# Kernel tuning notes

Hardware: AMD Instinct MI355X
Metric: run time of the kernel (lower is better)

Reference implementation:

```python
import jax, jax.numpy as jnp
import numpy as np

INPUT_SIZE = 128
OUTPUT_SIZE = 32
LIFTING_DIM = 512
BATCH = 32768


def setup_inputs() -> dict:
    key = jax.random.key(0)
    ks = jax.random.split(key, 7)
    x = jax.random.normal(ks[0], (BATCH, INPUT_SIZE), dtype=jnp.float32)
    # Linear(input_size, lifting_dim) with bias (torch layout: W [out, in])
    lim1 = 1.0 / np.sqrt(INPUT_SIZE)
    W1 = jax.random.uniform(ks[1], (LIFTING_DIM, INPUT_SIZE), jnp.float32, -lim1, lim1)
    b1 = jax.random.uniform(ks[2], (LIFTING_DIM,), jnp.float32, -lim1, lim1)
    # Linear(lifting_dim, output_size, bias=False)
    lim2 = 1.0 / np.sqrt(LIFTING_DIM)
    W2 = jax.random.uniform(ks[3], (OUTPUT_SIZE, LIFTING_DIM), jnp.float32, -lim2, lim2)
    # Quadratic params: L_vars ~ randn, b ~ randn, c ~ randn (as in module init)
    n_tril = LIFTING_DIM * (LIFTING_DIM + 1) // 2
    L_vars = jax.random.normal(ks[4], (n_tril,), dtype=jnp.float32)
    qb = jax.random.normal(ks[5], (LIFTING_DIM,), dtype=jnp.float32)
    qc = jax.random.normal(ks[6], (1,), dtype=jnp.float32)
    return {"x": x, "W1": W1, "b1": b1, "W2": W2, "L_vars": L_vars, "qb": qb, "qc": qc}


def reference(x, W1, b1, W2, L_vars, qb, qc):
    # lifting: phi = tanh(x @ W1^T + b1)   [B, lifting_dim]
    phi = jnp.tanh(x @ W1.T + b1)
    # actor: linear feedback (no bias)     [B, output_size]
    pi = phi @ W2.T
    # critic: quadratic form y = phi' Q phi + b' phi + c with Q = L L^T (PSD)
    rows, cols = jnp.tril_indices(LIFTING_DIM)  # row-major, same order as torch.tril_indices
    L = jnp.zeros((LIFTING_DIM, LIFTING_DIM), dtype=L_vars.dtype).at[rows, cols].set(L_vars)
    Q = L @ L.T
    # diag(phi @ Q @ phi.T) == sum((phi @ Q) * phi, axis=1)  -- O(B*d^2), same math
    y = jnp.sum((phi @ Q) * phi, axis=1) + phi @ qb + qc  # [B]
    vf = y[:, None]  # [B, 1]
    return pi, vf
```

## Files before the change

kernel.cpp:

```cpp
#include <hip/hip_runtime.h>
#include <hip/hip_bf16.h>
#include <stdint.h>

typedef short bf16x8 __attribute__((ext_vector_type(8)));
typedef float f32x4 __attribute__((ext_vector_type(4)));

#define DEVI static __device__ __forceinline__

constexpr int B_   = 32768;
constexpr int IN_  = 128;
constexpr int LF_  = 512;
constexpr int OUT_ = 32;
constexpr int NE_  = 48;

constexpr size_t OFF_XB  = 0;
constexpr size_t OFF_LT  = 8388608;
constexpr size_t OFF_W1  = OFF_LT + 524288;
constexpr size_t OFF_W2E = OFF_W1 + 131072;

DEVI void gl2lds16(const void* g, void* l) {
    __builtin_amdgcn_global_load_lds(
        (const __attribute__((address_space(1))) unsigned int*)g,
        (__attribute__((address_space(3))) unsigned int*)l,
        16, 0, 0);
}

DEVI bf16x8 frag4(const char* base, int row, int kofs) {
    int c = ((kofs >> 3) & 3) ^ (row & 3);
    return *(const bf16x8*)(base + (size_t)((row << 2) + c) * 16);
}
DEVI bf16x8 phiFrag(const char* p, int row, int kofs) {
    int c = (kofs >> 3) ^ (row & 7);
    return *(const bf16x8*)(p + (size_t)((row << 6) + c) * 16);
}
DEVI void phiStore(char* p, int row, int col, __hip_bfloat16 v) {
    int c = (col >> 3) ^ (row & 7);
    *(__hip_bfloat16*)(p + (size_t)((row << 6) + c) * 16 + (col & 7) * 2) = v;
}

__global__ __launch_bounds__(256) void k_prep(
        const float* __restrict__ x,  const float* __restrict__ w1,
        const float* __restrict__ w2, const float* __restrict__ lv,
        const float* __restrict__ qb,
        __hip_bfloat16* __restrict__ xb, __hip_bfloat16* __restrict__ w1b,
        __hip_bfloat16* __restrict__ lt, __hip_bfloat16* __restrict__ w2e) {
    int gt = blockIdx.x * blockDim.x + threadIdx.x;
    int st = gridDim.x * blockDim.x;
    for (int i = gt; i < B_ * IN_; i += st) xb[i] = __float2bfloat16(x[i]);
    for (int i = gt; i < LF_ * IN_; i += st) w1b[i] = __float2bfloat16(w1[i]);
    for (int i = gt; i < NE_ * LF_; i += st) {
        int n = i >> 9, k = i & 511;
        float v = (n < OUT_) ? w2[n * LF_ + k] : (n == OUT_ ? qb[k] : 0.f);
        w2e[i] = __float2bfloat16(v);
    }
    for (int i = gt; i < LF_ * LF_; i += st) {
        int j = i >> 9, k = i & 511;
        float v = (k >= j) ? lv[k * (k + 1) / 2 + j] : 0.f;
        lt[i] = __float2bfloat16(v);
    }
}

__global__ __launch_bounds__(256, 2) void k_fused(
        const __hip_bfloat16* __restrict__ xb, const __hip_bfloat16* __restrict__ w1b,
        const float* __restrict__ b1, const __hip_bfloat16* __restrict__ w2e,
        const __hip_bfloat16* __restrict__ lt, const float* __restrict__ qcp,
        float* __restrict__ pi, float* __restrict__ vf) {
    __shared__ char smem[79104];
    char*  phiB   = smem;
    char*  stageA = smem + 65536;
    char*  stageB = smem + 69632;
    float* vfb    = (float*)(smem + 77824);
    float* vfp    = (float*)(smem + 78080);

    const int tid = threadIdx.x, wv = tid >> 6, ln = tid & 63;
    const int cl = ln & 15, q = ln >> 4;
    const int m0 = blockIdx.x * 64;

    {
        const int wm = (wv & 1) * 32, wn = (wv >> 1) * 64;
        for (int n0 = 0; n0 < LF_; n0 += 128) {
            f32x4 acc[2][4] = {};
            for (int k0 = 0; k0 < IN_; k0 += 32) {
                __syncthreads();
                {
                    int slot = tid, row = slot >> 2, c = (slot & 3) ^ (row & 3);
                    gl2lds16(xb + (size_t)(m0 + row) * IN_ + k0 + c * 8,
                             stageA + (size_t)(wv * 64) * 16);
                }
#pragma unroll
                for (int it = 0; it < 2; ++it) {
                    int slot = it * 256 + tid, row = slot >> 2, c = (slot & 3) ^ (row & 3);
                    gl2lds16(w1b + (size_t)(n0 + row) * IN_ + k0 + c * 8,
                             stageB + (size_t)(it * 256 + wv * 64) * 16);
                }
                __syncthreads();
                bf16x8 af[2], bfr[4];
#pragma unroll
                for (int i = 0; i < 2; ++i) af[i]  = frag4(stageA, wm + i * 16 + cl, q * 8);
#pragma unroll
                for (int i = 0; i < 4; ++i) bfr[i] = frag4(stageB, wn + i * 16 + cl, q * 8);
#pragma unroll
                for (int mi = 0; mi < 2; ++mi)
#pragma unroll
                    for (int ni = 0; ni < 4; ++ni)
                        acc[mi][ni] = __builtin_amdgcn_mfma_f32_16x16x32_bf16(
                            af[mi], bfr[ni], acc[mi][ni], 0, 0, 0);
            }
#pragma unroll
            for (int ni = 0; ni < 4; ++ni) {
                int colg = n0 + wn + ni * 16 + cl;
                float bv = b1[colg];
#pragma unroll
                for (int mi = 0; mi < 2; ++mi)
#pragma unroll
                    for (int r = 0; r < 4; ++r) {
                        int row = wm + mi * 16 + q * 4 + r;
                        phiStore(phiB, row, colg,
                                 __float2bfloat16(tanhf(acc[mi][ni][r] + bv)));
                    }
            }
        }
    }
    __syncthreads();

    {
        const int wm = wv * 16;
        f32x4 a2[3] = {};
        for (int k0 = 0; k0 < LF_; k0 += 32) {
            bf16x8 a = phiFrag(phiB, wm + cl, k0 + q * 8);
#pragma unroll
            for (int ni = 0; ni < 3; ++ni) {
                bf16x8 b = *(const bf16x8*)(w2e + (size_t)(ni * 16 + cl) * LF_ + k0 + q * 8);
                a2[ni] = __builtin_amdgcn_mfma_f32_16x16x32_bf16(a, b, a2[ni], 0, 0, 0);
            }
        }
#pragma unroll
        for (int ni = 0; ni < 3; ++ni)
#pragma unroll
            for (int r = 0; r < 4; ++r) {
                int row = wm + q * 4 + r, col = ni * 16 + cl;
                float v = a2[ni][r];
                if (col < OUT_)       pi[(size_t)(m0 + row) * OUT_ + col] = v;
                else if (col == OUT_) vfb[row] = v;
            }
    }

    {
        const int wn = wv * 32;
        float vacc[4][4] = {};
        for (int n0 = 0; n0 < LF_; n0 += 128) {
            f32x4 acc[4][2] = {};
            for (int k0 = n0; k0 < LF_; k0 += 32) {
                __syncthreads();
#pragma unroll
                for (int it = 0; it < 2; ++it) {
                    int slot = it * 256 + tid, row = slot >> 2, c = (slot & 3) ^ (row & 3);
                    gl2lds16(lt + (size_t)(n0 + row) * LF_ + k0 + c * 8,
                             stageB + (size_t)(it * 256 + wv * 64) * 16);
                }
                __syncthreads();
                bf16x8 bfr[2];
#pragma unroll
                for (int ni = 0; ni < 2; ++ni) bfr[ni] = frag4(stageB, wn + ni * 16 + cl, q * 8);
#pragma unroll
                for (int mi = 0; mi < 4; ++mi) {
                    bf16x8 a = phiFrag(phiB, mi * 16 + cl, k0 + q * 8);
#pragma unroll
                    for (int ni = 0; ni < 2; ++ni)
                        acc[mi][ni] = __builtin_amdgcn_mfma_f32_16x16x32_bf16(
                            a, bfr[ni], acc[mi][ni], 0, 0, 0);
                }
            }
#pragma unroll
            for (int mi = 0; mi < 4; ++mi)
#pragma unroll
                for (int r = 0; r < 4; ++r) {
                    float s = 0.f;
#pragma unroll
                    for (int ni = 0; ni < 2; ++ni) { float t = acc[mi][ni][r]; s += t * t; }
                    vacc[mi][r] += s;
                }
        }
#pragma unroll
        for (int mi = 0; mi < 4; ++mi)
#pragma unroll
            for (int r = 0; r < 4; ++r) {
                float v = vacc[mi][r];
                v += __shfl_xor(v, 1, 64);
                v += __shfl_xor(v, 2, 64);
                v += __shfl_xor(v, 4, 64);
                v += __shfl_xor(v, 8, 64);
                vacc[mi][r] = v;
            }
        if (cl == 0)
#pragma unroll
            for (int mi = 0; mi < 4; ++mi)
#pragma unroll
                for (int r = 0; r < 4; ++r)
                    vfp[wv * 64 + mi * 16 + q * 4 + r] = vacc[mi][r];
    }
    __syncthreads();
    if (tid < 64) {
        float v = vfb[tid] + qcp[0] +
                  vfp[tid] + vfp[64 + tid] + vfp[128 + tid] + vfp[192 + tid];
        vf[m0 + tid] = v;
    }
}

extern "C" void kernel_launch(void* const* d_in, const int* in_sizes, int n_in,
                              void* d_out, int out_size, void* d_ws, size_t ws_size,
                              hipStream_t stream) {
    const float* x  = (const float*)d_in[0];
    const float* w1 = (const float*)d_in[1];
    const float* b1 = (const float*)d_in[2];
    const float* w2 = (const float*)d_in[3];
    const float* lv = (const float*)d_in[4];
    const float* qb = (const float*)d_in[5];
    const float* qc = (const float*)d_in[6];

    char* ws = (char*)d_ws;
    __hip_bfloat16* xb  = (__hip_bfloat16*)(ws + OFF_XB);
    __hip_bfloat16* lt  = (__hip_bfloat16*)(ws + OFF_LT);
    __hip_bfloat16* w1b = (__hip_bfloat16*)(ws + OFF_W1);
    __hip_bfloat16* w2e = (__hip_bfloat16*)(ws + OFF_W2E);

    float* pi = (float*)d_out;
    float* vf = pi + (size_t)B_ * OUT_;

    k_prep <<<1024, 256, 0, stream>>>(x, w1, w2, lv, qb, xb, w1b, lt, w2e);
    k_fused<<<B_ / 64, 256, 0, stream>>>(xb, w1b, b1, w2e, lt, qc, pi, vf);
}
```

Baseline: 128.2 us.

## Fuse x bf16 conversion into main kernel, drop LDS staging, rebalance triangular GEMM

The fp32-to-bf16 conversion of x now happens inside the fused kernel, which removes the 8 MB bf16 round-trip and shrinks the prep kernel to weights only. The prep kernel transposes L through a shared-memory tile so its reads and writes are coalesced. In the fused kernel the W1 and L operands are read straight from global/L2 into registers rather than staged through LDS with barriers, so most of the per-k __syncthreads are gone. Triangular tiles are dealt to waves in paired order to balance work, and tanh uses an exp/rcp approximation. The risks are more global-load latency exposed without LDS staging, and a small accuracy loss from the approximate tanh.

```diff
diff --git a/kernel.cpp b/kernel.cpp
--- a/kernel.cpp
+++ b/kernel.cpp
@@ -13,111 +13,124 @@
 constexpr int OUT_ = 32;
 constexpr int NE_  = 48;
 
-constexpr size_t OFF_XB  = 0;
-constexpr size_t OFF_LT  = 8388608;
-constexpr size_t OFF_W1  = OFF_LT + 524288;
+constexpr size_t OFF_LT  = 0;
+constexpr size_t OFF_W1  = 524288;
 constexpr size_t OFF_W2E = OFF_W1 + 131072;
 
-DEVI void gl2lds16(const void* g, void* l) {
-    __builtin_amdgcn_global_load_lds(
-        (const __attribute__((address_space(1))) unsigned int*)g,
-        (__attribute__((address_space(3))) unsigned int*)l,
-        16, 0, 0);
-}
-
-DEVI bf16x8 frag4(const char* base, int row, int kofs) {
-    int c = ((kofs >> 3) & 3) ^ (row & 3);
-    return *(const bf16x8*)(base + (size_t)((row << 2) + c) * 16);
-}
+DEVI short f2bs(float f) { __hip_bfloat16 h = __float2bfloat16(f); return *(short*)&h; }
+
+DEVI float tanh_fast(float v) {
+    float e = __expf(2.0f * v);
+    return 1.0f - 2.0f * __builtin_amdgcn_rcpf(e + 1.0f);
+}
+
 DEVI bf16x8 phiFrag(const char* p, int row, int kofs) {
     int c = (kofs >> 3) ^ (row & 7);
     return *(const bf16x8*)(p + (size_t)((row << 6) + c) * 16);
 }
-DEVI void phiStore(char* p, int row, int col, __hip_bfloat16 v) {
+DEVI void phiStore(char* p, int row, int col, float v) {
     int c = (col >> 3) ^ (row & 7);
-    *(__hip_bfloat16*)(p + (size_t)((row << 6) + c) * 16 + (col & 7) * 2) = v;
+    *(short*)(p + (size_t)((row << 6) + c) * 16 + (col & 7) * 2) = f2bs(v);
+}
+DEVI bf16x8 xFrag(const char* p, int row, int kofs) {
+    int c = (kofs >> 3) ^ (row & 15);
+    return *(const bf16x8*)(p + (size_t)((row << 4) + c) * 16);
 }
 
 __global__ __launch_bounds__(256) void k_prep(
-        const float* __restrict__ x,  const float* __restrict__ w1,
-        const float* __restrict__ w2, const float* __restrict__ lv,
-        const float* __restrict__ qb,
-        __hip_bfloat16* __restrict__ xb, __hip_bfloat16* __restrict__ w1b,
-        __hip_bfloat16* __restrict__ lt, __hip_bfloat16* __restrict__ w2e) {
-    int gt = blockIdx.x * blockDim.x + threadIdx.x;
-    int st = gridDim.x * blockDim.x;
-    for (int i = gt; i < B_ * IN_; i += st) xb[i] = __float2bfloat16(x[i]);
-    for (int i = gt; i < LF_ * IN_; i += st) w1b[i] = __float2bfloat16(w1[i]);
-    for (int i = gt; i < NE_ * LF_; i += st) {
-        int n = i >> 9, k = i & 511;
-        float v = (n < OUT_) ? w2[n * LF_ + k] : (n == OUT_ ? qb[k] : 0.f);
-        w2e[i] = __float2bfloat16(v);
-    }
-    for (int i = gt; i < LF_ * LF_; i += st) {
-        int j = i >> 9, k = i & 511;
-        float v = (k >= j) ? lv[k * (k + 1) / 2 + j] : 0.f;
-        lt[i] = __float2bfloat16(v);
+        const float* __restrict__ w1, const float* __restrict__ w2,
+        const float* __restrict__ lv, const float* __restrict__ qb,
+        __hip_bfloat16* __restrict__ w1b, __hip_bfloat16* __restrict__ lt,
+        __hip_bfloat16* __restrict__ w2e) {
+    int b = blockIdx.x, tid = threadIdx.x;
+    if (b < 64) {
+        __shared__ float tbuf[64][65];
+        int bj = b >> 3, bk = b & 7;
+        for (int i = tid; i < 4096; i += 256) {
+            int kk = i >> 6, jj = i & 63;
+            int k = bk * 64 + kk, j = bj * 64 + jj;
+            tbuf[kk][jj] = (k >= j) ? lv[k * (k + 1) / 2 + j] : 0.f;
+        }
+        __syncthreads();
+        for (int i = tid; i < 4096; i += 256) {
+            int jj = i >> 6, kk = i & 63;
+            lt[(size_t)(bj * 64 + jj) * LF_ + bk * 64 + kk] = __float2bfloat16(tbuf[kk][jj]);
+        }
+    } else if (b < 96) {
+        int gt = (b - 64) * 256 + tid;
+        for (int i = gt; i < LF_ * IN_ / 4; i += 8192) {
+            float4 v = ((const float4*)w1)[i];
+            short4 s = { f2bs(v.x), f2bs(v.y), f2bs(v.z), f2bs(v.w) };
+            ((short4*)w1b)[i] = s;
+        }
+    } else {
+        int gt = (b - 96) * 256 + tid;
+        for (int i = gt; i < NE_ * LF_; i += 8192) {
+            int n = i >> 9, k = i & 511;
+            float v = (n < OUT_) ? w2[n * LF_ + k] : (n == OUT_ ? qb[k] : 0.f);
+            w2e[i] = __float2bfloat16(v);
+        }
     }
 }
 
 __global__ __launch_bounds__(256, 2) void k_fused(
-        const __hip_bfloat16* __restrict__ xb, const __hip_bfloat16* __restrict__ w1b,
+        const float* __restrict__ x, const __hip_bfloat16* __restrict__ w1b,
         const float* __restrict__ b1, const __hip_bfloat16* __restrict__ w2e,
         const __hip_bfloat16* __restrict__ lt, const float* __restrict__ qcp,
         float* __restrict__ pi, float* __restrict__ vf) {
-    __shared__ char smem[79104];
-    char*  phiB   = smem;
-    char*  stageA = smem + 65536;
-    char*  stageB = smem + 69632;
-    float* vfb    = (float*)(smem + 77824);
-    float* vfp    = (float*)(smem + 78080);
+    __shared__ char smem[81920];
+    char*  phiB  = smem;
+    char*  stage = smem + 65536;
+    float* vfb   = (float*)stage;
+    float* vfp   = (float*)(stage + 256);
 
     const int tid = threadIdx.x, wv = tid >> 6, ln = tid & 63;
     const int cl = ln & 15, q = ln >> 4;
     const int m0 = blockIdx.x * 64;
 
+#pragma unroll
+    for (int it = 0; it < 4; ++it) {
+        int slot = it * 256 + tid, row = slot >> 4, cg = slot & 15;
+        const float4* p = (const float4*)(x + (size_t)(m0 + row) * IN_ + cg * 8);
+        float4 u0 = p[0], u1 = p[1];
+        bf16x8 pk;
+        pk[0] = f2bs(u0.x); pk[1] = f2bs(u0.y); pk[2] = f2bs(u0.z); pk[3] = f2bs(u0.w);
+        pk[4] = f2bs(u1.x); pk[5] = f2bs(u1.y); pk[6] = f2bs(u1.z); pk[7] = f2bs(u1.w);
+        *(bf16x8*)(stage + (size_t)((row << 4) + (cg ^ (row & 15))) * 16) = pk;
+    }
+    __syncthreads();
+
     {
-        const int wm = (wv & 1) * 32, wn = (wv >> 1) * 64;
-        for (int n0 = 0; n0 < LF_; n0 += 128) {
-            f32x4 acc[2][4] = {};
+        const int n0w = wv * 128;
+#pragma unroll
+        for (int ch = 0; ch < 2; ++ch) {
+            f32x4 acc[4][4] = {};
+#pragma unroll
             for (int k0 = 0; k0 < IN_; k0 += 32) {
-                __syncthreads();
-                {
-                    int slot = tid, row = slot >> 2, c = (slot & 3) ^ (row & 3);
-                    gl2lds16(xb + (size_t)(m0 + row) * IN_ + k0 + c * 8,
-                             stageA + (size_t)(wv * 64) * 16);
-                }
-#pragma unroll
-                for (int it = 0; it < 2; ++it) {
-                    int slot = it * 256 + tid, row = slot >> 2, c = (slot & 3) ^ (row & 3);
-                    gl2lds16(w1b + (size_t)(n0 + row) * IN_ + k0 + c * 8,
-                             stageB + (size_t)(it * 256 + wv * 64) * 16);
-                }
-                __syncthreads();
-                bf16x8 af[2], bfr[4];
-#pragma unroll
-                for (int i = 0; i < 2; ++i) af[i]  = frag4(stageA, wm + i * 16 + cl, q * 8);
-#pragma unroll
-                for (int i = 0; i < 4; ++i) bfr[i] = frag4(stageB, wn + i * 16 + cl, q * 8);
-#pragma unroll
-                for (int mi = 0; mi < 2; ++mi)
+                bf16x8 a[4], bfr[4];
+#pragma unroll
+                for (int mi = 0; mi < 4; ++mi) a[mi] = xFrag(stage, mi * 16 + cl, k0 + q * 8);
+#pragma unroll
+                for (int ni = 0; ni < 4; ++ni)
+                    bfr[ni] = *(const bf16x8*)(
+                        w1b + (size_t)(n0w + ch * 64 + ni * 16 + cl) * IN_ + k0 + q * 8);
+#pragma unroll
+                for (int mi = 0; mi < 4; ++mi)
 #pragma unroll
                     for (int ni = 0; ni < 4; ++ni)
                         acc[mi][ni] = __builtin_amdgcn_mfma_f32_16x16x32_bf16(
-                            af[mi], bfr[ni], acc[mi][ni], 0, 0, 0);
+                            a[mi], bfr[ni], acc[mi][ni], 0, 0, 0);
             }
 #pragma unroll
             for (int ni = 0; ni < 4; ++ni) {
-                int colg = n0 + wn + ni * 16 + cl;
+                int colg = n0w + ch * 64 + ni * 16 + cl;
                 float bv = b1[colg];
 #pragma unroll
-                for (int mi = 0; mi < 2; ++mi)
-#pragma unroll
-                    for (int r = 0; r < 4; ++r) {
-                        int row = wm + mi * 16 + q * 4 + r;
-                        phiStore(phiB, row, colg,
-                                 __float2bfloat16(tanhf(acc[mi][ni][r] + bv)));
-                    }
+                for (int mi = 0; mi < 4; ++mi)
+#pragma unroll
+                    for (int r = 0; r < 4; ++r)
+                        phiStore(phiB, mi * 16 + q * 4 + r, colg,
+                                 tanh_fast(acc[mi][ni][r] + bv));
             }
         }
     }
@@ -146,40 +159,40 @@
     }
 
     {
-        const int wn = wv * 32;
         float vacc[4][4] = {};
-        for (int n0 = 0; n0 < LF_; n0 += 128) {
-            f32x4 acc[4][2] = {};
-            for (int k0 = n0; k0 < LF_; k0 += 32) {
-                __syncthreads();
-#pragma unroll
-                for (int it = 0; it < 2; ++it) {
-                    int slot = it * 256 + tid, row = slot >> 2, c = (slot & 3) ^ (row & 3);
-                    gl2lds16(lt + (size_t)(n0 + row) * LF_ + k0 + c * 8,
-                             stageB + (size_t)(it * 256 + wv * 64) * 16);
+#pragma unroll
+        for (int s = 0; s < 2; ++s) {
+            int tl[4] = { 16 * s + wv, 16 * s + 7 - wv, 16 * s + 8 + wv, 16 * s + 15 - wv };
+            int ks[4];
+#pragma unroll
+            for (int j = 0; j < 4; ++j) ks[j] = (tl[j] * 16) & ~31;
+            int kmin = min(min(ks[0], ks[1]), min(ks[2], ks[3]));
+            f32x4 acc[4][4] = {};
+            for (int k0 = kmin; k0 < LF_; k0 += 32) {
+                bf16x8 a[4];
+#pragma unroll
+                for (int mi = 0; mi < 4; ++mi) a[mi] = phiFrag(phiB, mi * 16 + cl, k0 + q * 8);
+#pragma unroll
+                for (int j = 0; j < 4; ++j) {
+                    if (k0 >= ks[j]) {
+                        bf16x8 b = *(const bf16x8*)(
+                            lt + (size_t)(tl[j] * 16 + cl) * LF_ + k0 + q * 8);
+#pragma unroll
+                        for (int mi = 0; mi < 4; ++mi)
+                            acc[j][mi] = __builtin_amdgcn_mfma_f32_16x16x32_bf16(
+                                a[mi], b, acc[j][mi], 0, 0, 0);
+                    }
                 }
-                __syncthreads();
-                bf16x8 bfr[2];
-#pragma unroll
-                for (int ni = 0; ni < 2; ++ni) bfr[ni] = frag4(stageB, wn + ni * 16 + cl, q * 8);
-#pragma unroll
-                for (int mi = 0; mi < 4; ++mi) {
-                    bf16x8 a = phiFrag(phiB, mi * 16 + cl, k0 + q * 8);
-#pragma unroll
-                    for (int ni = 0; ni < 2; ++ni)
-                        acc[mi][ni] = __builtin_amdgcn_mfma_f32_16x16x32_bf16(
-                            a, bfr[ni], acc[mi][ni], 0, 0, 0);
-                }
-            }
-#pragma unroll
-            for (int mi = 0; mi < 4; ++mi)
-#pragma unroll
-                for (int r = 0; r < 4; ++r) {
-                    float s = 0.f;
-#pragma unroll
-                    for (int ni = 0; ni < 2; ++ni) { float t = acc[mi][ni][r]; s += t * t; }
-                    vacc[mi][r] += s;
-                }
+            }
+#pragma unroll
+            for (int j = 0; j < 4; ++j)
+#pragma unroll
+                for (int mi = 0; mi < 4; ++mi)
+#pragma unroll
+                    for (int r = 0; r < 4; ++r) {
+                        float t = acc[j][mi][r];
+                        vacc[mi][r] += t * t;
+                    }
         }
 #pragma unroll
         for (int mi = 0; mi < 4; ++mi)
@@ -200,11 +213,9 @@
                     vfp[wv * 64 + mi * 16 + q * 4 + r] = vacc[mi][r];
     }
     __syncthreads();
-    if (tid < 64) {
-        float v = vfb[tid] + qcp[0] +
-                  vfp[tid] + vfp[64 + tid] + vfp[128 + tid] + vfp[192 + tid];
-        vf[m0 + tid] = v;
-    }
+    if (tid < 64)
+        vf[m0 + tid] = vfb[tid] + qcp[0] +
+                       vfp[tid] + vfp[64 + tid] + vfp[128 + tid] + vfp[192 + tid];
 }
 
 extern "C" void kernel_launch(void* const* d_in, const int* in_sizes, int n_in,
@@ -219,7 +230,6 @@
     const float* qc = (const float*)d_in[6];
 
     char* ws = (char*)d_ws;
-    __hip_bfloat16* xb  = (__hip_bfloat16*)(ws + OFF_XB);
     __hip_bfloat16* lt  = (__hip_bfloat16*)(ws + OFF_LT);
     __hip_bfloat16* w1b = (__hip_bfloat16*)(ws + OFF_W1);
     __hip_bfloat16* w2e = (__hip_bfloat16*)(ws + OFF_W2E);
@@ -227,6 +237,6 @@
     float* pi = (float*)d_out;
     float* vf = pi + (size_t)B_ * OUT_;
 
-    k_prep <<<1024, 256, 0, stream>>>(x, w1, w2, lv, qb, xb, w1b, lt, w2e);
-    k_fused<<<B_ / 64, 256, 0, stream>>>(xb, w1b, b1, w2e, lt, qc, pi, vf);
-}
+    k_prep <<<128, 256, 0, stream>>>(w1, w2, lv, qb, w1b, lt, w2e);
+    k_fused<<<B_ / 64, 256, 0, stream>>>(x, w1b, b1, w2e, lt, qc, pi, vf);
+}
```

Result: faster. 123.4 us (-3.7%).
